# Optimization experiments

Measured on AMD Instinct MI355X. Metric: run time of the kernel, lower is better.

## Reference

```python
import jax, jax.numpy as jnp
import numpy as np
import math

B, T, N, D = 2, 2048, 16, 128


def setup_inputs() -> dict:
    key = jax.random.key(0)
    ks = jax.random.split(key, 9)
    s = 1.0 / math.sqrt(D)
    return {
        "x": jax.random.normal(ks[0], (B, T, N, D), dtype=jnp.float32),
        "wq": jax.random.normal(ks[1], (D, D), dtype=jnp.float32) * s,
        "bq": jax.random.normal(ks[2], (D,), dtype=jnp.float32) * 0.02,
        "wk": jax.random.normal(ks[3], (D, D), dtype=jnp.float32) * s,
        "bk": jax.random.normal(ks[4], (D,), dtype=jnp.float32) * 0.02,
        "wv": jax.random.normal(ks[5], (D, D), dtype=jnp.float32) * s,
        "bv": jax.random.normal(ks[6], (D,), dtype=jnp.float32) * 0.02,
        "wp": jax.random.normal(ks[7], (D, D), dtype=jnp.float32) * s,
        "bp": jax.random.normal(ks[8], (D,), dtype=jnp.float32) * 0.02,
    }


def reference(x, wq, bq, wk, bk, wv, bv, wp, bp):
    # x: (B, T, N, D); per-head Linear projections (torch y = x @ W.T + b)
    d = x.shape[-1]
    q = jnp.einsum("btnd,ed->btne", x, wq) + bq  # (B,T,N,D)
    k = jnp.einsum("btnd,ed->btne", x, wk) + bk
    v = jnp.einsum("btnd,ed->btne", x, wv) + bv
    scale = 1.0 / jnp.sqrt(jnp.asarray(d, dtype=x.dtype))
    # scores: (B, N, T, T)
    scores = jnp.einsum("btnd,bsnd->bnts", q, k) * scale
    t = scores.shape[-1]
    causal = jnp.tril(jnp.ones((t, t), dtype=bool))  # (T,T)
    scores = jnp.where(causal[None, None], scores, jnp.asarray(-jnp.inf, scores.dtype))
    w = jax.nn.softmax(scores, axis=-1)
    att = jnp.einsum("bnts,bsnd->btnd", w, v)  # (B,T,N,D)
    out = jnp.einsum("btnd,ed->btne", att, wp) + bp
    return out
```

## Files before the change

### kernel.cpp

```cpp
#include <hip/hip_runtime.h>
#include <cmath>

#define BB 2
#define TT 2048
#define NN 16
#define DD 128
#define NROWS (BB*TT*NN)
#define PLANE (TT*DD)
#define KP 132
#define VP 68
#define TP 129

typedef unsigned short u16;
typedef unsigned int   u32;
typedef __attribute__((ext_vector_type(8)))  short s8v;
typedef __attribute__((ext_vector_type(16))) float vf16;

__device__ u16 g_Q [(size_t)NROWS * DD];
__device__ u16 g_K [(size_t)NROWS * DD];
__device__ u16 g_VT[(size_t)NROWS * DD];

__device__ __forceinline__ u16 f2bf(float f) {
    return (u16)((__float_as_uint(f) + 0x8000u) >> 16);
}
__device__ __forceinline__ u32 pk2(float a, float b) {
    return ((__float_as_uint(a) + 0x8000u) >> 16)
         | ((__float_as_uint(b) + 0x8000u) & 0xFFFF0000u);
}
__device__ __forceinline__ void st8(u16* p, const float4& a, const float4& b) {
    uint2 lo, hi;
    lo.x = pk2(a.x, a.y); lo.y = pk2(a.z, a.w);
    hi.x = pk2(b.x, b.y); hi.y = pk2(b.z, b.w);
    *(uint2*)p       = lo;
    *(uint2*)(p + 4) = hi;
}
__device__ __forceinline__ s8v ld8(const u16* p) {
    short4 a = *(const short4*)p;
    short4 b = *(const short4*)(p + 4);
    return (s8v){a.x, a.y, a.z, a.w, b.x, b.y, b.z, b.w};
}

__device__ __forceinline__ void bar_lds()
{
    asm volatile("s_waitcnt lgkmcnt(0)" ::: "memory");
    __builtin_amdgcn_sched_barrier(0);
    __builtin_amdgcn_s_barrier();
    __builtin_amdgcn_sched_barrier(0);
}

__global__ __launch_bounds__(256)
void qkv_proj_kernel(const float* __restrict__ x,
                     const float* __restrict__ Wq, const float* __restrict__ Bq,
                     const float* __restrict__ Wk, const float* __restrict__ Bk,
                     const float* __restrict__ Wv, const float* __restrict__ Bv)
{
    __shared__ u16 Xs[128*KP];
    __shared__ u16 Ws[128*KP];

    const int t    = threadIdx.x;
    const int bnp  = blockIdx.x >> 4;
    const int tt0  = (blockIdx.x & 15) * 128;
    const size_t xrow0 = ((size_t)((bnp >> 4)*TT + tt0)*NN + (bnp & 15)) * DD;

    #pragma unroll
    for (int it = 0; it < 8; ++it) {
        int i = t + 256*it;
        int e = i >> 4, c8 = i & 15;
        const float* xp = x + xrow0 + (size_t)e*(NN*DD) + c8*8;
        st8(&Xs[e*KP + c8*8], *(const float4*)xp, *(const float4*)(xp + 4));
    }
    #pragma unroll
    for (int it = 0; it < 8; ++it) {
        int i = t + 256*it;
        int e = i >> 4, c8 = i & 15;
        st8(&Ws[e*KP + c8*8], ((const float4*)Wq)[2*i], ((const float4*)Wq)[2*i + 1]);
    }
    __syncthreads();

    const int w   = t >> 6;
    const int l31 = t & 31;
    const int q2  = (t >> 5) & 1;

    s8v af[8];
    #pragma unroll
    for (int s = 0; s < 8; ++s)
        af[s] = ld8(&Xs[(w*32 + l31)*KP + s*16 + q2*8]);

    uint2 wl[8], wh[8];

    #pragma unroll
    for (int wsel = 0; wsel < 3; ++wsel) {
        const float* Bi = (wsel == 0) ? Bq : (wsel == 1) ? Bk : Bv;

        if (wsel < 2) {
            const float* Wn = (wsel == 0) ? Wk : Wv;
            #pragma unroll
            for (int it = 0; it < 8; ++it) {
                int i = t + 256*it;
                float4 a = ((const float4*)Wn)[2*i];
                float4 b = ((const float4*)Wn)[2*i + 1];
                wl[it].x = pk2(a.x, a.y); wl[it].y = pk2(a.z, a.w);
                wh[it].x = pk2(b.x, b.y); wh[it].y = pk2(b.z, b.w);
            }
        }

        vf16 acc[4];
        #pragma unroll
        for (int et = 0; et < 4; ++et)
            #pragma unroll
            for (int i = 0; i < 16; ++i) acc[et][i] = 0.f;

        #pragma unroll
        for (int s = 0; s < 8; ++s) {
            #pragma unroll
            for (int et = 0; et < 4; ++et) {
                s8v bf = ld8(&Ws[(et*32 + l31)*KP + s*16 + q2*8]);
                acc[et] = __builtin_amdgcn_mfma_f32_32x32x16_bf16(af[s], bf, acc[et], 0, 0, 0);
            }
        }

        float bb[4];
        #pragma unroll
        for (int et = 0; et < 4; ++et) bb[et] = Bi[et*32 + l31];

        if (wsel < 2) {
            u16* Ot = (wsel == 0) ? g_Q : g_K;
            #pragma unroll
            for (int r = 0; r < 16; ++r) {
                int rl = (r & 3) + 8*(r >> 2) + 4*q2;
                size_t orow = (size_t)bnp*PLANE + (size_t)(tt0 + w*32 + rl)*DD;
                #pragma unroll
                for (int et = 0; et < 4; ++et) {
                    float ov = acc[et][r] + bb[et];
                    if (wsel == 0) ov *= 0.12752053685940512f;
                    Ot[orow + et*32 + l31] = f2bf(ov);
                }
            }
            __syncthreads();
            #pragma unroll
            for (int it = 0; it < 8; ++it) {
                int i = t + 256*it;
                int e = i >> 4, c8 = i & 15;
                *(uint2*)&Ws[e*KP + c8*8]     = wl[it];
                *(uint2*)&Ws[e*KP + c8*8 + 4] = wh[it];
            }
            __syncthreads();
        } else {
            u16* Xt = (u16*)Xs;
            #pragma unroll
            for (int r = 0; r < 16; ++r) {
                int rl = (r & 3) + 8*(r >> 2) + 4*q2;
                int row = w*32 + rl;
                #pragma unroll
                for (int et = 0; et < 4; ++et)
                    Xt[row*TP + et*32 + l31] = f2bf(acc[et][r] + bb[et]);
            }
            __syncthreads();
            const size_t vbase = (size_t)bnp*PLANE + tt0;
            #pragma unroll
            for (int c = 0; c < 8; ++c) {
                int idx = t + 256*c;
                int d = idx >> 4, tc = idx & 15;
                u16 e8[8];
                #pragma unroll
                for (int i = 0; i < 8; ++i) e8[i] = Xt[(tc*8 + i)*TP + d];
                uint4 pkv;
                pkv.x = (u32)e8[0] | ((u32)e8[1] << 16);
                pkv.y = (u32)e8[2] | ((u32)e8[3] << 16);
                pkv.z = (u32)e8[4] | ((u32)e8[5] << 16);
                pkv.w = (u32)e8[6] | ((u32)e8[7] << 16);
                *(uint4*)&g_VT[vbase + (size_t)d*TT + tc*8] = pkv;
            }
        }
    }
}

__global__ __launch_bounds__(256, 2)
void attn_kernel(const float* __restrict__ Wp, const float* __restrict__ Bp,
                 float* __restrict__ out)
{
    __shared__ u16 Ks[2][64*KP];
    __shared__ u16 Vt[2][128*VP];

    const int t   = threadIdx.x;
    const int grp = blockIdx.x >> 5;
    const int bn  = blockIdx.x & 31;
    const int qt  = (grp < 8) ? (15 - grp) : (grp - 8);
    const int q0  = qt * 128;
    const size_t plane = (size_t)bn * PLANE;
    const u16* Kg = g_K  + plane;
    const u16* Vg = g_VT + plane;

    const int w      = t >> 6;
    const int lane   = t & 63;
    const int lane31 = lane & 31;
    const int q2     = lane >> 5;
    const int qband  = q0 + 32*w;
    const int qrow   = qband + lane31;

    s8v qf[8];
    {
        const u16* Qg = g_Q + plane + (size_t)qrow * DD;
        #pragma unroll
        for (int s = 0; s < 8; ++s)
            qf[s] = *(const s8v*)&Qg[s*16 + q2*8];
    }

    vf16 accO[4];
    #pragma unroll
    for (int dt = 0; dt < 4; ++dt)
        #pragma unroll
        for (int i = 0; i < 16; ++i) accO[dt][i] = 0.f;

    float lrow = 0.f;
    const int nkt = 2*qt + 2;

    uint4 pk[4], pv[4];

    auto LOADT = [&](int kt) {
        const u16* K2 = Kg + (size_t)(kt*64)*DD;
        const u16* V2 = Vg + kt*64;
        #pragma unroll
        for (int c = 0; c < 4; ++c) {
            int j = t + 256*c;
            int kr = j >> 4, kc = j & 15;
            pk[c] = *(const uint4*)&K2[kr*DD + kc*8];
            int vr = j >> 3, vc = j & 7;
            pv[c] = *(const uint4*)&V2[(size_t)vr*TT + vc*8];
        }
    };
    auto STORET = [&](int buf) {
        #pragma unroll
        for (int c = 0; c < 4; ++c) {
            int j = t + 256*c;
            int kr = j >> 4, kc = j & 15;
            uint2 a, b;
            a.x = pk[c].x; a.y = pk[c].y; b.x = pk[c].z; b.y = pk[c].w;
            *(uint2*)&Ks[buf][kr*KP + kc*8]     = a;
            *(uint2*)&Ks[buf][kr*KP + kc*8 + 4] = b;
            int vr = j >> 3, vc = j & 7;
            a.x = pv[c].x; a.y = pv[c].y; b.x = pv[c].z; b.y = pv[c].w;
            *(uint2*)&Vt[buf][vr*VP + vc*8]     = a;
            *(uint2*)&Vt[buf][vr*VP + vc*8 + 4] = b;
        }
    };

    LOADT(0);
    STORET(0);
    LOADT(1);

    for (int kt = 0; kt < nkt; ++kt) {
        const int k0 = kt*64;
        const int cb = kt & 1;
        bar_lds();

        if (kt + 1 < nkt) {
            STORET(cb ^ 1);
            if (kt + 2 < nkt) LOADT(kt + 2);
        }

        if (k0 <= qband + 31) {
            const u16* Kb = Ks[cb];
            const u16* Vb = Vt[cb];

            vf16 accS[2];
            #pragma unroll
            for (int kk = 0; kk < 2; ++kk)
                #pragma unroll
                for (int i = 0; i < 16; ++i) accS[kk][i] = 0.f;
            __builtin_amdgcn_s_setprio(1);
            #pragma unroll
            for (int s = 0; s < 8; ++s) {
                #pragma unroll
                for (int kk = 0; kk < 2; ++kk) {
                    s8v a = ld8(&Kb[(kk*32 + lane31)*KP + s*16 + q2*8]);
                    accS[kk] = __builtin_amdgcn_mfma_f32_32x32x16_bf16(a, qf[s], accS[kk], 0, 0, 0);
                }
            }
            __builtin_amdgcn_s_setprio(0);

            float p[2][16];
            const bool tail = (k0 + 63 > qband);
            #pragma unroll
            for (int kk = 0; kk < 2; ++kk)
                #pragma unroll
                for (int r = 0; r < 16; ++r) {
                    float sv = accS[kk][r];
                    if (tail) {
                        int keyg = k0 + kk*32 + (r & 3) + 8*(r >> 2) + 4*q2;
                        if (keyg > qrow) sv = -INFINITY;
                    }
                    p[kk][r] = sv;
                }

            float ls0 = 0.f, ls1 = 0.f;
            #pragma unroll
            for (int r = 0; r < 16; ++r) {
                float e0 = __builtin_amdgcn_exp2f(p[0][r] - 16.f);
                float e1 = __builtin_amdgcn_exp2f(p[1][r] - 16.f);
                p[0][r] = e0; p[1][r] = e1;
                ls0 += e0; ls1 += e1;
            }
            float ls = ls0 + ls1;
            ls += __shfl_xor(ls, 32);
            lrow += ls;

            s8v pf[4];
            #pragma unroll
            for (int tau = 0; tau < 4; ++tau) {
                int kk = tau >> 1, rb = (tau & 1)*8;
                s8v v;
                #pragma unroll
                for (int j = 0; j < 8; ++j)
                    v[j] = (short)(__float_as_uint(p[kk][rb + j]) >> 16);
                pf[tau] = v;
            }

            __builtin_amdgcn_s_setprio(1);
            #pragma unroll
            for (int dt = 0; dt < 4; ++dt) {
                const u16* vp = &Vb[(dt*32 + lane31)*VP];
                #pragma unroll
                for (int tau = 0; tau < 4; ++tau) {
                    const u16* q = vp + 16*tau + 4*q2;
                    short4 lo = *(const short4*)q;
                    short4 hi = *(const short4*)(q + 8);
                    s8v bvv = {lo.x, lo.y, lo.z, lo.w, hi.x, hi.y, hi.z, hi.w};
                    accO[dt] = __builtin_amdgcn_mfma_f32_32x32x16_bf16(pf[tau], bvv, accO[dt], 0, 0, 0);
                }
            }
            __builtin_amdgcn_s_setprio(0);
        }
    }

    bar_lds();
    u16* Os  = &Ks[0][0];
    u16* Wps = &Vt[0][0];

    {
        float inv = 1.0f / lrow;
        #pragma unroll
        for (int r = 0; r < 16; ++r) {
            int rl = (r & 3) + 8*(r >> 2) + 4*q2;
            float ir = __shfl(inv, rl);
            u16* op = &Os[(32*w + rl)*KP];
            #pragma unroll
            for (int dt = 0; dt < 4; ++dt)
                op[dt*32 + lane31] = f2bf(accO[dt][r] * ir);
        }
    }
    #pragma unroll
    for (int it = 0; it < 8; ++it) {
        int i = t + 256*it;
        int e = i >> 4, c8 = i & 15;
        st8(&Wps[e*KP + c8*8], ((const float4*)Wp)[2*i], ((const float4*)Wp)[2*i + 1]);
    }
    bar_lds();

    {
        s8v af[8];
        #pragma unroll
        for (int s = 0; s < 8; ++s)
            af[s] = ld8(&Os[(w*32 + lane31)*KP + s*16 + q2*8]);

        vf16 acc[4];
        #pragma unroll
        for (int et = 0; et < 4; ++et)
            #pragma unroll
            for (int i = 0; i < 16; ++i) acc[et][i] = 0.f;

        #pragma unroll
        for (int s = 0; s < 8; ++s) {
            #pragma unroll
            for (int et = 0; et < 4; ++et) {
                s8v bf = ld8(&Wps[(et*32 + lane31)*KP + s*16 + q2*8]);
                acc[et] = __builtin_amdgcn_mfma_f32_32x32x16_bf16(af[s], bf, acc[et], 0, 0, 0);
            }
        }

        float bb[4];
        #pragma unroll
        for (int et = 0; et < 4; ++et) bb[et] = Bp[et*32 + lane31];

        const int b = bn >> 4, n = bn & 15;
        #pragma unroll
        for (int r = 0; r < 16; ++r) {
            int rl = (r & 3) + 8*(r >> 2) + 4*q2;
            int qg = q0 + w*32 + rl;
            size_t orow = ((size_t)(b*TT + qg)*NN + n) * DD;
            #pragma unroll
            for (int et = 0; et < 4; ++et)
                out[orow + et*32 + lane31] = acc[et][r] + bb[et];
        }
    }
}

extern "C" void kernel_launch(void* const* d_in, const int* in_sizes, int n_in,
                              void* d_out, int out_size, void* d_ws, size_t ws_size,
                              hipStream_t stream)
{
    const float* x  = (const float*)d_in[0];
    const float* wq = (const float*)d_in[1];
    const float* bq = (const float*)d_in[2];
    const float* wk = (const float*)d_in[3];
    const float* bk = (const float*)d_in[4];
    const float* wv = (const float*)d_in[5];
    const float* bv = (const float*)d_in[6];
    const float* wp = (const float*)d_in[7];
    const float* bp = (const float*)d_in[8];
    float* out = (float*)d_out;
    (void)d_ws; (void)ws_size;

    qkv_proj_kernel<<<dim3(NROWS/128), dim3(256), 0, stream>>>(
        x, wq, bq, wk, bk, wv, bv);
    attn_kernel<<<dim3(BB*NN*(TT/128)), dim3(256), 0, stream>>>(wp, bp, out);
}
```

Before: 172.7 us.

## Halve QKV projection tile and stage Q/K outputs through LDS for coalesced stores

The QKV projection kernel now handles 64 sequence rows per block instead of 128, which doubles the grid. The four waves are split into a 2x2 row/column arrangement, so each wave computes half the output columns. Q and K results are first written to a padded LDS tile and then copied to global memory as 16-byte coalesced rows, replacing the scattered 2-byte global stores. The costs are an extra LDS round trip and barrier, and each block now reloads the weight matrices for half as many rows.

```diff
diff --git a/kernel.cpp b/kernel.cpp
--- a/kernel.cpp
+++ b/kernel.cpp
@@ -9,6 +9,7 @@
 #define PLANE (TT*DD)
 #define KP 132
 #define VP 68
+#define BP 136
 #define TP 129
 
 typedef unsigned short u16;
@@ -54,16 +55,16 @@
                      const float* __restrict__ Wk, const float* __restrict__ Bk,
                      const float* __restrict__ Wv, const float* __restrict__ Bv)
 {
-    __shared__ u16 Xs[128*KP];
+    __shared__ u16 Xs[64*BP];
     __shared__ u16 Ws[128*KP];
 
     const int t    = threadIdx.x;
-    const int bnp  = blockIdx.x >> 4;
-    const int tt0  = (blockIdx.x & 15) * 128;
+    const int bnp  = blockIdx.x >> 5;
+    const int tt0  = (blockIdx.x & 31) * 64;
     const size_t xrow0 = ((size_t)((bnp >> 4)*TT + tt0)*NN + (bnp & 15)) * DD;
 
     #pragma unroll
-    for (int it = 0; it < 8; ++it) {
+    for (int it = 0; it < 4; ++it) {
         int i = t + 256*it;
         int e = i >> 4, c8 = i & 15;
         const float* xp = x + xrow0 + (size_t)e*(NN*DD) + c8*8;
@@ -78,13 +79,15 @@
     __syncthreads();
 
     const int w   = t >> 6;
+    const int rh  = w >> 1;
+    const int ch  = w & 1;
     const int l31 = t & 31;
     const int q2  = (t >> 5) & 1;
 
     s8v af[8];
     #pragma unroll
     for (int s = 0; s < 8; ++s)
-        af[s] = ld8(&Xs[(w*32 + l31)*KP + s*16 + q2*8]);
+        af[s] = ld8(&Xs[(rh*32 + l31)*KP + s*16 + q2*8]);
 
     uint2 wl[8], wh[8];
 
@@ -104,39 +107,38 @@
             }
         }
 
-        vf16 acc[4];
-        #pragma unroll
-        for (int et = 0; et < 4; ++et)
+        vf16 acc[2];
+        #pragma unroll
+        for (int et = 0; et < 2; ++et)
             #pragma unroll
             for (int i = 0; i < 16; ++i) acc[et][i] = 0.f;
 
         #pragma unroll
         for (int s = 0; s < 8; ++s) {
             #pragma unroll
-            for (int et = 0; et < 4; ++et) {
-                s8v bf = ld8(&Ws[(et*32 + l31)*KP + s*16 + q2*8]);
+            for (int et = 0; et < 2; ++et) {
+                s8v bf = ld8(&Ws[(ch*64 + et*32 + l31)*KP + s*16 + q2*8]);
                 acc[et] = __builtin_amdgcn_mfma_f32_32x32x16_bf16(af[s], bf, acc[et], 0, 0, 0);
             }
         }
 
-        float bb[4];
-        #pragma unroll
-        for (int et = 0; et < 4; ++et) bb[et] = Bi[et*32 + l31];
+        float bb[2];
+        #pragma unroll
+        for (int et = 0; et < 2; ++et) bb[et] = Bi[ch*64 + et*32 + l31];
 
         if (wsel < 2) {
-            u16* Ot = (wsel == 0) ? g_Q : g_K;
+            __syncthreads();
             #pragma unroll
             for (int r = 0; r < 16; ++r) {
                 int rl = (r & 3) + 8*(r >> 2) + 4*q2;
-                size_t orow = (size_t)bnp*PLANE + (size_t)(tt0 + w*32 + rl)*DD;
-                #pragma unroll
-                for (int et = 0; et < 4; ++et) {
+                int row = rh*32 + rl;
+                #pragma unroll
+                for (int et = 0; et < 2; ++et) {
                     float ov = acc[et][r] + bb[et];
                     if (wsel == 0) ov *= 0.12752053685940512f;
-                    Ot[orow + et*32 + l31] = f2bf(ov);
+                    Xs[row*BP + ch*64 + et*32 + l31] = f2bf(ov);
                 }
             }
-            __syncthreads();
             #pragma unroll
             for (int it = 0; it < 8; ++it) {
                 int i = t + 256*it;
@@ -145,25 +147,33 @@
                 *(uint2*)&Ws[e*KP + c8*8 + 4] = wh[it];
             }
             __syncthreads();
+            u16* Ot = ((wsel == 0) ? g_Q : g_K) + (size_t)bnp*PLANE + (size_t)tt0*DD;
+            #pragma unroll
+            for (int c = 0; c < 4; ++c) {
+                int j = t + 256*c;
+                int row = j >> 4, c8 = j & 15;
+                uint4 v = *(const uint4*)&Xs[row*BP + c8*8];
+                *(uint4*)&Ot[row*DD + c8*8] = v;
+            }
         } else {
-            u16* Xt = (u16*)Xs;
+            __syncthreads();
             #pragma unroll
             for (int r = 0; r < 16; ++r) {
                 int rl = (r & 3) + 8*(r >> 2) + 4*q2;
-                int row = w*32 + rl;
-                #pragma unroll
-                for (int et = 0; et < 4; ++et)
-                    Xt[row*TP + et*32 + l31] = f2bf(acc[et][r] + bb[et]);
+                int row = rh*32 + rl;
+                #pragma unroll
+                for (int et = 0; et < 2; ++et)
+                    Xs[row*TP + ch*64 + et*32 + l31] = f2bf(acc[et][r] + bb[et]);
             }
             __syncthreads();
             const size_t vbase = (size_t)bnp*PLANE + tt0;
             #pragma unroll
-            for (int c = 0; c < 8; ++c) {
+            for (int c = 0; c < 4; ++c) {
                 int idx = t + 256*c;
-                int d = idx >> 4, tc = idx & 15;
+                int d = idx >> 3, tc = idx & 7;
                 u16 e8[8];
                 #pragma unroll
-                for (int i = 0; i < 8; ++i) e8[i] = Xt[(tc*8 + i)*TP + d];
+                for (int i = 0; i < 8; ++i) e8[i] = Xs[(tc*8 + i)*TP + d];
                 uint4 pkv;
                 pkv.x = (u32)e8[0] | ((u32)e8[1] << 16);
                 pkv.y = (u32)e8[2] | ((u32)e8[3] << 16);
@@ -411,7 +421,7 @@
     float* out = (float*)d_out;
     (void)d_ws; (void)ws_size;
 
-    qkv_proj_kernel<<<dim3(NROWS/128), dim3(256), 0, stream>>>(
+    qkv_proj_kernel<<<dim3(BB*NN*32), dim3(256), 0, stream>>>(
         x, wq, bq, wk, bk, wv, bv);
     attn_kernel<<<dim3(BB*NN*(TT/128)), dim3(256), 0, stream>>>(wp, bp, out);
 }
```

Result: slower. 178.8 us (+3.5%).
